# Optimization experiments

Measured on AMD Instinct MI355X. Metric: run time of the kernel, lower is better.

Reference implementation:

```python
import jax, jax.numpy as jnp
import numpy as np

L = 2       # num_layers
D = 256     # d_model
DFF = 1024  # d_ffn
NH = 8      # n_heads
NP = 4      # n_points
CIN = 512   # in_channels
B = 8
HH = 64
WW = 64
EPS = 1e-5


def setup_inputs() -> dict:
    key = jax.random.key(0)
    ks = iter(jax.random.split(key, 48))
    def w(shape, s=0.02):
        return jax.random.normal(next(ks), shape, jnp.float32) * s
    inp = dict(
        x=jax.random.normal(next(ks), (B, CIN, HH, WW), jnp.float32),
        W_in=w((D, CIN)),
        bn1_g=jnp.ones((D,), jnp.float32), bn1_b=jnp.zeros((D,), jnp.float32),
        bn1_m=jnp.zeros((D,), jnp.float32), bn1_v=jnp.ones((D,), jnp.float32),
        query_embed=w((HH * WW, D), 1.0),
        Woff=w((L, D, NH * NP * 2)), boff=w((L, NH * NP * 2), 2.0),
        Wattn=w((L, D, NH * NP)), battn=jnp.zeros((L, NH * NP), jnp.float32),
        Wval=w((L, D, D)), bval=jnp.zeros((L, D), jnp.float32),
        Wo=w((L, D, D)), bo=jnp.zeros((L, D), jnp.float32),
        ln1_g=jnp.ones((L, D), jnp.float32), ln1_b=jnp.zeros((L, D), jnp.float32),
        W1=w((L, D, DFF)), b1=jnp.zeros((L, DFF), jnp.float32),
        W2=w((L, DFF, D)), b2=jnp.zeros((L, D), jnp.float32),
        ln2_g=jnp.ones((L, D), jnp.float32), ln2_b=jnp.zeros((L, D), jnp.float32),
        W_out=w((CIN, D)),
        bn2_g=jnp.ones((CIN,), jnp.float32), bn2_b=jnp.zeros((CIN,), jnp.float32),
        bn2_m=jnp.zeros((CIN,), jnp.float32), bn2_v=jnp.ones((CIN,), jnp.float32),
    )
    return inp


def layer_norm(x, g, b):
    m = jnp.mean(x, axis=-1, keepdims=True)
    v = jnp.mean((x - m) ** 2, axis=-1, keepdims=True)
    return (x - m) * jax.lax.rsqrt(v + EPS) * g + b


def bilinear_sample(value, loc, Hh, Ww):
    # value: (B, NH, dh, H*W); loc: (B, Lq, NH, NP, 2) normalized to [0,1]
    # Matches F.grid_sample(align_corners=False, padding_mode='zeros') with grid=2*loc-1.
    Bn, Lq, nH, P, _ = loc.shape
    gx = loc[..., 0] * Ww - 0.5
    gy = loc[..., 1] * Hh - 0.5
    x0 = jnp.floor(gx)
    y0 = jnp.floor(gy)
    wx = gx - x0
    wy = gy - y0
    x0i = x0.astype(jnp.int32)
    y0i = y0.astype(jnp.int32)

    def t(a):  # (B,Lq,NH,P) -> (B,NH,1,Lq*P)
        return jnp.transpose(a, (0, 2, 1, 3)).reshape(Bn, nH, 1, Lq * P)

    def gather(xi, yi):
        valid = (xi >= 0) & (xi < Ww) & (yi >= 0) & (yi < Hh)
        xc = jnp.clip(xi, 0, Ww - 1)
        yc = jnp.clip(yi, 0, Hh - 1)
        idx = t(yc * Ww + xc)  # (B,NH,1,Lq*P)
        v = jnp.take_along_axis(value, idx, axis=3)  # (B,NH,dh,Lq*P)
        return v * t(valid).astype(value.dtype)

    v00 = gather(x0i, y0i)
    v10 = gather(x0i + 1, y0i)
    v01 = gather(x0i, y0i + 1)
    v11 = gather(x0i + 1, y0i + 1)
    wxt = t(wx)
    wyt = t(wy)
    out = (v00 * (1 - wxt) * (1 - wyt) + v10 * wxt * (1 - wyt)
           + v01 * (1 - wxt) * wyt + v11 * wxt * wyt)
    return out.reshape(Bn, nH, -1, Lq, P)  # (B,NH,dh,Lq,NP)


def reference(x, W_in, bn1_g, bn1_b, bn1_m, bn1_v, query_embed,
              Woff, boff, Wattn, battn, Wval, bval, Wo, bo,
              ln1_g, ln1_b, W1, b1, W2, b2, ln2_g, ln2_b,
              W_out, bn2_g, bn2_b, bn2_m, bn2_v):
    Bn, C, Hh, Ww = x.shape
    HW = Hh * Ww
    dh = D // NH

    # proj_in: 1x1 conv (no bias) + BN (inference) + ReLU
    xp = jnp.einsum('bchw,dc->bdhw', x, W_in)
    xp = (xp - bn1_m[:, None, None]) * jax.lax.rsqrt(bn1_v[:, None, None] + EPS)
    xp = jax.nn.relu(xp * bn1_g[:, None, None] + bn1_b[:, None, None])
    src = xp.reshape(Bn, D, HW).transpose(0, 2, 1)  # (B, HW, D)

    # reference points: centers of pixels, normalized
    ry = (jnp.arange(Hh, dtype=jnp.float32) + 0.5) / Hh
    rx = (jnp.arange(Ww, dtype=jnp.float32) + 0.5) / Ww
    yy, xx = jnp.meshgrid(ry, rx, indexing='ij')
    refpts = jnp.stack([xx, yy], axis=-1).reshape(HW, 2)  # (HW, 2) as (x, y)
    norm = jnp.array([Ww, Hh], jnp.float32)

    q = jnp.broadcast_to(query_embed[None], (Bn, HW, D))
    for i in range(L):
        # --- MSDeformAttn (n_levels=1) ---
        val = (src @ Wval[i] + bval[i]).reshape(Bn, HW, NH, dh)
        val = val.transpose(0, 2, 3, 1)  # (B, NH, dh, HW)
        off = (q @ Woff[i] + boff[i]).reshape(Bn, HW, NH, NP, 2)
        attn = jax.nn.softmax((q @ Wattn[i] + battn[i]).reshape(Bn, HW, NH, NP), axis=-1)
        loc = refpts[None, :, None, None, :] + off / norm  # (B, HW, NH, NP, 2)
        samp = bilinear_sample(val, loc, Hh, Ww)  # (B, NH, dh, HW, NP)
        o = jnp.einsum('bhdqp,bhqp->bqhd', samp, attn.transpose(0, 2, 1, 3))
        o = o.reshape(Bn, HW, D) @ Wo[i] + bo[i]
        q = layer_norm(q + o, ln1_g[i], ln1_b[i])
        # --- FFN ---
        ffn = jax.nn.relu(q @ W1[i] + b1[i]) @ W2[i] + b2[i]
        q = layer_norm(q + ffn, ln2_g[i], ln2_b[i])

    # proj_out: 1x1 conv (no bias) + BN (inference) + ReLU
    y = q.transpose(0, 2, 1).reshape(Bn, D, Hh, Ww)
    y = jnp.einsum('bdhw,cd->bchw', y, W_out)
    y = (y - bn2_m[:, None, None]) * jax.lax.rsqrt(bn2_v[:, None, None] + EPS)
    return jax.nn.relu(y * bn2_g[:, None, None] + bn2_b[:, None, None])
```

## Files before the change

kernel.cpp:

```cpp
#include <hip/hip_runtime.h>
#include <cstdint>

#define LYR 2
#define DM  256
#define DFFN 1024
#define CINC 512
#define BBATCH 8
#define HWTOT 4096
#define EPSV 1e-5f

using u16 = unsigned short;
typedef __attribute__((ext_vector_type(8))) short bf16x8;
typedef __attribute__((ext_vector_type(4))) float f32x4;

__device__ inline u16 f2b(float v) {
    union { float f; uint32_t u; } x; x.f = v;
    uint32_t r = x.u + 0x7fffu + ((x.u >> 16) & 1u);
    return (u16)(r >> 16);
}
__device__ inline uint32_t pk2(float a, float b) {
    return (uint32_t)f2b(a) | ((uint32_t)f2b(b) << 16);
}
__device__ inline float blo(uint32_t d) {
    union { uint32_t i; float f; } x; x.i = d << 16; return x.f;
}
__device__ inline float bhi(uint32_t d) {
    union { uint32_t i; float f; } x; x.i = d & 0xffff0000u; return x.f;
}

template<int MODE>
__global__ __launch_bounds__(256) void mfma_gemm(
    const u16* __restrict__ A, const u16* __restrict__ Bt,
    const float* __restrict__ scale, const float* __restrict__ shift,
    void* __restrict__ Cv, int M, int N, int K, int ldc,
    long long a_zs, long long b_zs, long long c_zs, int swz, int gxlog)
{
    __shared__ u16 As[4][4096];
    __shared__ u16 Bs[4][4096];
    const int tid = threadIdx.x;
    const int lane = tid & 63;
    const int wid = tid >> 6;
    const int wm = (wid & 1) << 6, wn = (wid >> 1) << 6;
    const int quad = lane >> 4, r = lane & 15;

    int bx = blockIdx.x, by = blockIdx.y;
    if (swz) {
        int linear = by * gridDim.x + bx;
        int xcd = linear & 7;
        int s = linear >> 3;
        bx = s & (gridDim.x - 1);
        by = xcd * (gridDim.y >> 3) + (s >> gxlog);
    }
    const int m0 = by << 7, n0 = bx << 7;
    const u16* Ab = A + (long long)blockIdx.z * a_zs + (long long)m0 * K;
    const u16* Bb = Bt + (long long)blockIdx.z * b_zs + (long long)n0 * K;

    const int u0 = tid, u1 = tid + 256;
    const int mu0 = u0 >> 2, cu0 = (u0 & 3) ^ ((mu0 >> 1) & 3);
    const int mu1 = u1 >> 2, cu1 = (u1 & 3) ^ ((mu1 >> 1) & 3);
    const long long ga0 = (long long)mu0 * K + cu0 * 8;
    const long long ga1 = (long long)mu1 * K + cu1 * 8;

    int aoff[4], boff[4];
#pragma unroll
    for (int t = 0; t < 4; ++t) {
        int m = wm + t * 16 + r;
        aoff[t] = (m * 4 + (quad ^ ((m >> 1) & 3))) * 8;
        int n = wn + t * 16 + r;
        boff[t] = (n * 4 + (quad ^ ((n >> 1) & 3))) * 8;
    }

    f32x4 acc[4][4];
#pragma unroll
    for (int i = 0; i < 4; ++i)
#pragma unroll
        for (int j = 0; j < 4; ++j) acc[i][j] = (f32x4){0.f, 0.f, 0.f, 0.f};

    const int NT = K >> 5;

#define GSTAGE(g, b) do {                                                                       \
    const long long kk = (long long)(g) << 5;                                                   \
    __builtin_amdgcn_global_load_lds((const __attribute__((address_space(1))) void*)(Ab + ga0 + kk), \
        (__attribute__((address_space(3))) void*)(&As[b][u0 * 8]), 16, 0, 0);                   \
    __builtin_amdgcn_global_load_lds((const __attribute__((address_space(1))) void*)(Ab + ga1 + kk), \
        (__attribute__((address_space(3))) void*)(&As[b][u1 * 8]), 16, 0, 0);                   \
    __builtin_amdgcn_global_load_lds((const __attribute__((address_space(1))) void*)(Bb + ga0 + kk), \
        (__attribute__((address_space(3))) void*)(&Bs[b][u0 * 8]), 16, 0, 0);                   \
    __builtin_amdgcn_global_load_lds((const __attribute__((address_space(1))) void*)(Bb + ga1 + kk), \
        (__attribute__((address_space(3))) void*)(&Bs[b][u1 * 8]), 16, 0, 0);                   \
} while (0)

    GSTAGE(0, 0);
    GSTAGE(1, 1);
    GSTAGE(2, 2);

    for (int t = 0; t < NT; ++t) {
        if (t < NT - 2)       asm volatile("s_waitcnt vmcnt(8)" ::: "memory");
        else if (t == NT - 2) asm volatile("s_waitcnt vmcnt(4)" ::: "memory");
        else                  asm volatile("s_waitcnt vmcnt(0)" ::: "memory");
        __builtin_amdgcn_s_barrier();
        __builtin_amdgcn_sched_barrier(0);
        if (t + 3 < NT) GSTAGE(t + 3, (t + 3) & 3);
        const u16* Ap = As[t & 3];
        const u16* Bp = Bs[t & 3];
        bf16x8 af[4], bf[4];
#pragma unroll
        for (int tt = 0; tt < 4; ++tt) af[tt] = *(const bf16x8*)(Ap + aoff[tt]);
#pragma unroll
        for (int tt = 0; tt < 4; ++tt) bf[tt] = *(const bf16x8*)(Bp + boff[tt]);
#pragma unroll
        for (int i = 0; i < 4; ++i)
#pragma unroll
            for (int j = 0; j < 4; ++j)
                acc[i][j] = __builtin_amdgcn_mfma_f32_16x16x32_bf16(bf[j], af[i], acc[i][j], 0, 0, 0);
    }
#undef GSTAGE

    const long long zc = (long long)blockIdx.z * c_zs;
    float4 sh4[4], sc4[4];
    if (MODE != 3) {
#pragma unroll
        for (int j = 0; j < 4; ++j) {
            int colb = n0 + wn + j * 16 + quad * 4;
            sh4[j] = *(const float4*)&shift[colb];
            if (MODE == 1) sc4[j] = *(const float4*)&scale[colb];
        }
    }
#pragma unroll
    for (int i = 0; i < 4; ++i) {
        const int row = m0 + wm + i * 16 + r;
        float rsc = 0.f, rsh = 0.f;
        if (MODE == 3) { rsc = scale[row]; rsh = shift[row]; }
#pragma unroll
        for (int j = 0; j < 4; ++j) {
            const int colb = n0 + wn + j * 16 + quad * 4;
            f32x4 v = acc[i][j];
            if (MODE == 0) {
                uint2 o;
                o.x = pk2(v[0] + sh4[j].x, v[1] + sh4[j].y);
                o.y = pk2(v[2] + sh4[j].z, v[3] + sh4[j].w);
                *(uint2*)((u16*)Cv + zc + (long long)row * ldc + colb) = o;
            } else if (MODE == 1) {
                uint2 o;
                o.x = pk2(fmaxf(v[0] * sc4[j].x + sh4[j].x, 0.f), fmaxf(v[1] * sc4[j].y + sh4[j].y, 0.f));
                o.y = pk2(fmaxf(v[2] * sc4[j].z + sh4[j].z, 0.f), fmaxf(v[3] * sc4[j].w + sh4[j].w, 0.f));
                *(uint2*)((u16*)Cv + zc + (long long)row * ldc + colb) = o;
            } else if (MODE == 2) {
                float4 o = {v[0] + sh4[j].x, v[1] + sh4[j].y, v[2] + sh4[j].z, v[3] + sh4[j].w};
                *(float4*)((float*)Cv + zc + (long long)row * ldc + colb) = o;
            } else {
                float4 o = {fmaxf(v[0] * rsc + rsh, 0.f), fmaxf(v[1] * rsc + rsh, 0.f),
                            fmaxf(v[2] * rsc + rsh, 0.f), fmaxf(v[3] * rsc + rsh, 0.f)};
                *(float4*)((float*)Cv + zc + (long long)row * ldc + colb) = o;
            }
        }
    }
}

__global__ __launch_bounds__(512, 4) void mfma_gemm_ln(
    const u16* __restrict__ A, const u16* __restrict__ Bf,
    const float* __restrict__ bias,
    float* __restrict__ q, u16* __restrict__ q16,
    const float* __restrict__ g, const float* __restrict__ beta, int K)
{
    __shared__ u16 As[3][2048];
    __shared__ float red_s[8][64], red_ss[8][64];
    const int tid = threadIdx.x;
    const int lane = tid & 63;
    const int w = tid >> 6;
    const int quad = lane >> 4, r = lane & 15;
    const int m0 = blockIdx.x << 6;
    const u16* Ab = A + (long long)m0 * K;

    const int mA = tid >> 2, cA = (tid & 3) ^ ((mA >> 1) & 3);
    const long long gaA = (long long)mA * K + cA * 8;
    const bool stager = tid < 256;

    int aoff[4];
#pragma unroll
    for (int t = 0; t < 4; ++t) {
        int m = t * 16 + r;
        aoff[t] = (m * 4 + (quad ^ ((m >> 1) & 3))) * 8;
    }

    const u16* Bw = Bf + ((size_t)(2 * w) * 64 + lane) * 8;

    f32x4 acc[4][2];
#pragma unroll
    for (int i = 0; i < 4; ++i)
#pragma unroll
        for (int j = 0; j < 2; ++j) acc[i][j] = (f32x4){0.f, 0.f, 0.f, 0.f};

    const int NT = K >> 5;

    if (stager) {
        __builtin_amdgcn_global_load_lds((const __attribute__((address_space(1))) void*)(Ab + gaA),
                                         (__attribute__((address_space(3))) void*)(&As[0][tid * 8]), 16, 0, 0);
        __builtin_amdgcn_global_load_lds((const __attribute__((address_space(1))) void*)(Ab + gaA + 32),
                                         (__attribute__((address_space(3))) void*)(&As[1][tid * 8]), 16, 0, 0);
    }
    __builtin_amdgcn_sched_barrier(0);
    bf16x8 bc0 = *(const bf16x8*)(Bw);
    bf16x8 bc1 = *(const bf16x8*)(Bw + 512);

    int cb = 0;
    for (int t = 0; t < NT; ++t) {
        asm volatile("s_waitcnt vmcnt(3)" ::: "memory");
        __builtin_amdgcn_s_barrier();
        __builtin_amdgcn_sched_barrier(0);
        int nb = cb + 2; if (nb >= 3) nb -= 3;
        if (stager && t + 2 < NT)
            __builtin_amdgcn_global_load_lds((const __attribute__((address_space(1))) void*)(Ab + gaA + (long long)(t + 2) * 32),
                                             (__attribute__((address_space(3))) void*)(&As[nb][tid * 8]), 16, 0, 0);
        bf16x8 bn0, bn1;
        if (t + 1 < NT) {
            const u16* Bn = Bw + (size_t)(t + 1) * 8192;
            bn0 = *(const bf16x8*)(Bn);
            bn1 = *(const bf16x8*)(Bn + 512);
        } else { bn0 = bc0; bn1 = bc1; }

        const u16* Ac = As[cb];
        bf16x8 af[4];
#pragma unroll
        for (int tt = 0; tt < 4; ++tt) af[tt] = *(const bf16x8*)(Ac + aoff[tt]);
#pragma unroll
        for (int i = 0; i < 4; ++i) {
            acc[i][0] = __builtin_amdgcn_mfma_f32_16x16x32_bf16(bc0, af[i], acc[i][0], 0, 0, 0);
            acc[i][1] = __builtin_amdgcn_mfma_f32_16x16x32_bf16(bc1, af[i], acc[i][1], 0, 0, 0);
        }
        bc0 = bn0; bc1 = bn1;
        cb = (cb + 1 == 3) ? 0 : cb + 1;
    }

    float4 sh2[2];
#pragma unroll
    for (int j = 0; j < 2; ++j)
        sh2[j] = *(const float4*)&bias[w * 32 + j * 16 + quad * 4];

    float s_[4] = {0.f, 0.f, 0.f, 0.f}, ss_[4] = {0.f, 0.f, 0.f, 0.f};
#pragma unroll
    for (int i = 0; i < 4; ++i) {
        const int row = m0 + i * 16 + r;
#pragma unroll
        for (int j = 0; j < 2; ++j) {
            const int colb = w * 32 + j * 16 + quad * 4;
            float4 qo = *(const float4*)&q[(size_t)row * DM + colb];
            acc[i][j][0] += sh2[j].x + qo.x;
            acc[i][j][1] += sh2[j].y + qo.y;
            acc[i][j][2] += sh2[j].z + qo.z;
            acc[i][j][3] += sh2[j].w + qo.w;
#pragma unroll
            for (int e = 0; e < 4; ++e) {
                s_[i] += acc[i][j][e];
                ss_[i] += acc[i][j][e] * acc[i][j][e];
            }
        }
    }
#pragma unroll
    for (int i = 0; i < 4; ++i) {
        s_[i] += __shfl_xor(s_[i], 16);  ss_[i] += __shfl_xor(ss_[i], 16);
        s_[i] += __shfl_xor(s_[i], 32);  ss_[i] += __shfl_xor(ss_[i], 32);
    }
    if (quad == 0) {
#pragma unroll
        for (int i = 0; i < 4; ++i) {
            red_s[w][i * 16 + r] = s_[i];
            red_ss[w][i * 16 + r] = ss_[i];
        }
    }
    __syncthreads();

    float mean[4], rstd[4];
#pragma unroll
    for (int i = 0; i < 4; ++i) {
        float S = 0.f, SS = 0.f;
#pragma unroll
        for (int w2 = 0; w2 < 8; ++w2) { S += red_s[w2][i * 16 + r]; SS += red_ss[w2][i * 16 + r]; }
        mean[i] = S * (1.0f / 256.0f);
        rstd[i] = rsqrtf(SS * (1.0f / 256.0f) - mean[i] * mean[i] + EPSV);
    }

    float4 g4[2], bt4[2];
#pragma unroll
    for (int j = 0; j < 2; ++j) {
        int colb = w * 32 + j * 16 + quad * 4;
        g4[j] = *(const float4*)&g[colb];
        bt4[j] = *(const float4*)&beta[colb];
    }
#pragma unroll
    for (int i = 0; i < 4; ++i) {
        const int row = m0 + i * 16 + r;
#pragma unroll
        for (int j = 0; j < 2; ++j) {
            const int colb = w * 32 + j * 16 + quad * 4;
            float o0 = (acc[i][j][0] - mean[i]) * rstd[i] * g4[j].x + bt4[j].x;
            float o1 = (acc[i][j][1] - mean[i]) * rstd[i] * g4[j].y + bt4[j].y;
            float o2 = (acc[i][j][2] - mean[i]) * rstd[i] * g4[j].z + bt4[j].z;
            float o3 = (acc[i][j][3] - mean[i]) * rstd[i] * g4[j].w + bt4[j].w;
            *(float4*)&q[(size_t)row * DM + colb] = make_float4(o0, o1, o2, o3);
            *(uint2*)(q16 + (size_t)row * DM + colb) = make_uint2(pk2(o0, o1), pk2(o2, o3));
        }
    }
}

__global__ __launch_bounds__(512) void ffn_fused(
    const u16* __restrict__ q16in, const u16* __restrict__ w1F, const u16* __restrict__ w2F,
    const float* __restrict__ b1, const float* __restrict__ b2,
    float* __restrict__ q, u16* __restrict__ q16,
    const float* __restrict__ g, const float* __restrict__ beta)
{
    __shared__ u16 Aq[16384];
    __shared__ u16 hF[16384];
    __shared__ float red_s[8][64], red_ss[8][64];
    const int tid = threadIdx.x;
    const int lane = tid & 63;
    const int w = tid >> 6;
    const int quad = lane >> 4, r = lane & 15;
    const int m0 = blockIdx.x << 6;

    const u16* Ab = q16in + (long long)m0 * DM;
#pragma unroll
    for (int i = 0; i < 4; ++i) {
        int u = tid + i * 512;
        int ks = u >> 8, v = u & 255;
        int m = v >> 2, c = (v & 3) ^ ((m >> 1) & 3);
        __builtin_amdgcn_global_load_lds((const __attribute__((address_space(1))) void*)(Ab + (long long)m * DM + ks * 32 + c * 8),
                                         (__attribute__((address_space(3))) void*)(Aq + u * 8), 16, 0, 0);
    }

    int aoff[4];
#pragma unroll
    for (int t = 0; t < 4; ++t) {
        int m = t * 16 + r;
        aoff[t] = (m * 4 + (quad ^ ((m >> 1) & 3))) * 8;
    }

    f32x4 acc2[4][2];
#pragma unroll
    for (int i = 0; i < 4; ++i)
#pragma unroll
        for (int j = 0; j < 2; ++j) acc2[i][j] = (f32x4){0.f, 0.f, 0.f, 0.f};

    __syncthreads();

    for (int qq = 0; qq < 4; ++qq) {
        f32x4 acc1[4][2];
#pragma unroll
        for (int i = 0; i < 4; ++i)
#pragma unroll
            for (int j = 0; j < 2; ++j) acc1[i][j] = (f32x4){0.f, 0.f, 0.f, 0.f};
        __builtin_amdgcn_s_setprio(1);
#pragma unroll
        for (int ks = 0; ks < 8; ++ks) {
            const u16* bp = w1F + ((size_t)(ks * 64 + qq * 16 + w * 2) * 64 + lane) * 8;
            bf16x8 bf0 = *(const bf16x8*)bp;
            bf16x8 bf1 = *(const bf16x8*)(bp + 512);
            bf16x8 af[4];
#pragma unroll
            for (int t = 0; t < 4; ++t) af[t] = *(const bf16x8*)(Aq + ks * 2048 + aoff[t]);
#pragma unroll
            for (int i = 0; i < 4; ++i) {
                acc1[i][0] = __builtin_amdgcn_mfma_f32_16x16x32_bf16(bf0, af[i], acc1[i][0], 0, 0, 0);
                acc1[i][1] = __builtin_amdgcn_mfma_f32_16x16x32_bf16(bf1, af[i], acc1[i][1], 0, 0, 0);
            }
        }
        __builtin_amdgcn_s_setprio(0);
        __syncthreads();

#pragma unroll
        for (int j = 0; j < 2; ++j) {
            const int cb = qq * 256 + w * 32 + j * 16 + quad * 4;
            const float4 b14 = *(const float4*)&b1[cb];
            const int lane2 = r | (((j * 2 + (quad >> 1)) & 3) << 4);
            const int eo = (quad & 1) * 4;
#pragma unroll
            for (int i = 0; i < 4; ++i) {
                f32x4 v = acc1[i][j];
                uint2 o;
                o.x = pk2(fmaxf(v[0] + b14.x, 0.f), fmaxf(v[1] + b14.y, 0.f));
                o.y = pk2(fmaxf(v[2] + b14.z, 0.f), fmaxf(v[3] + b14.w, 0.f));
                *(uint2*)(hF + ((w * 4 + i) * 64 + lane2) * 8 + eo) = o;
            }
        }
        __syncthreads();

        __builtin_amdgcn_s_setprio(1);
#pragma unroll
        for (int ks = 0; ks < 8; ++ks) {
            const u16* bp = w2F + ((size_t)((qq * 8 + ks) * 16 + w * 2) * 64 + lane) * 8;
            bf16x8 bf0 = *(const bf16x8*)bp;
            bf16x8 bf1 = *(const bf16x8*)(bp + 512);
            bf16x8 af[4];
#pragma unroll
            for (int t = 0; t < 4; ++t) af[t] = *(const bf16x8*)(hF + ((ks * 4 + t) * 64 + lane) * 8);
#pragma unroll
            for (int i = 0; i < 4; ++i) {
                acc2[i][0] = __builtin_amdgcn_mfma_f32_16x16x32_bf16(bf0, af[i], acc2[i][0], 0, 0, 0);
                acc2[i][1] = __builtin_amdgcn_mfma_f32_16x16x32_bf16(bf1, af[i], acc2[i][1], 0, 0, 0);
            }
        }
        __builtin_amdgcn_s_setprio(0);
    }

    float4 sh2[2];
#pragma unroll
    for (int j = 0; j < 2; ++j)
        sh2[j] = *(const float4*)&b2[w * 32 + j * 16 + quad * 4];

    float s_[4] = {0.f, 0.f, 0.f, 0.f}, ss_[4] = {0.f, 0.f, 0.f, 0.f};
#pragma unroll
    for (int i = 0; i < 4; ++i) {
        const int row = m0 + i * 16 + r;
#pragma unroll
        for (int j = 0; j < 2; ++j) {
            const int colb = w * 32 + j * 16 + quad * 4;
            float4 qo = *(const float4*)&q[(size_t)row * DM + colb];
            acc2[i][j][0] += sh2[j].x + qo.x;
            acc2[i][j][1] += sh2[j].y + qo.y;
            acc2[i][j][2] += sh2[j].z + qo.z;
            acc2[i][j][3] += sh2[j].w + qo.w;
#pragma unroll
            for (int e = 0; e < 4; ++e) {
                s_[i] += acc2[i][j][e];
                ss_[i] += acc2[i][j][e] * acc2[i][j][e];
            }
        }
    }
#pragma unroll
    for (int i = 0; i < 4; ++i) {
        s_[i] += __shfl_xor(s_[i], 16);  ss_[i] += __shfl_xor(ss_[i], 16);
        s_[i] += __shfl_xor(s_[i], 32);  ss_[i] += __shfl_xor(ss_[i], 32);
    }
    if (quad == 0) {
#pragma unroll
        for (int i = 0; i < 4; ++i) {
            red_s[w][i * 16 + r] = s_[i];
            red_ss[w][i * 16 + r] = ss_[i];
        }
    }
    __syncthreads();

    float mean[4], rstd[4];
#pragma unroll
    for (int i = 0; i < 4; ++i) {
        float S = 0.f, SS = 0.f;
#pragma unroll
        for (int w2 = 0; w2 < 8; ++w2) { S += red_s[w2][i * 16 + r]; SS += red_ss[w2][i * 16 + r]; }
        mean[i] = S * (1.0f / 256.0f);
        rstd[i] = rsqrtf(SS * (1.0f / 256.0f) - mean[i] * mean[i] + EPSV);
    }

    float4 g4[2], bt4[2];
#pragma unroll
    for (int j = 0; j < 2; ++j) {
        int colb = w * 32 + j * 16 + quad * 4;
        g4[j] = *(const float4*)&g[colb];
        bt4[j] = *(const float4*)&beta[colb];
    }
#pragma unroll
    for (int i = 0; i < 4; ++i) {
        const int row = m0 + i * 16 + r;
#pragma unroll
        for (int j = 0; j < 2; ++j) {
            const int colb = w * 32 + j * 16 + quad * 4;
            float o0 = (acc2[i][j][0] - mean[i]) * rstd[i] * g4[j].x + bt4[j].x;
            float o1 = (acc2[i][j][1] - mean[i]) * rstd[i] * g4[j].y + bt4[j].y;
            float o2 = (acc2[i][j][2] - mean[i]) * rstd[i] * g4[j].z + bt4[j].z;
            float o3 = (acc2[i][j][3] - mean[i]) * rstd[i] * g4[j].w + bt4[j].w;
            *(float4*)&q[(size_t)row * DM + colb] = make_float4(o0, o1, o2, o3);
            *(uint2*)(q16 + (size_t)row * DM + colb) = make_uint2(pk2(o0, o1), pk2(o2, o3));
        }
    }
}

__device__ __attribute__((noinline)) void tconv(const float* src, u16* dst, int K, int N, int tk, int tn)
{
    __shared__ float t[32][33];
    const int tx = threadIdx.x & 31, ty = threadIdx.x >> 5;
#pragma unroll
    for (int i = 0; i < 4; ++i)
        t[ty + i * 8][tx] = src[(size_t)(tk * 32 + ty + i * 8) * N + tn * 32 + tx];
    __syncthreads();
#pragma unroll
    for (int i = 0; i < 4; ++i)
        dst[(size_t)(tn * 32 + ty + i * 8) * K + tk * 32 + tx] = f2b(t[tx][ty + i * 8]);
}

__device__ __attribute__((noinline)) void tconv_oa(const float* Woff, const float* Wattn, u16* dst, int tk, int tn)
{
    __shared__ float t[32][33];
    const int tx = threadIdx.x & 31, ty = threadIdx.x >> 5;
#pragma unroll
    for (int i = 0; i < 4; ++i) {
        int k = tk * 32 + ty + i * 8, n = tn * 32 + tx;
        float v = (n < 64) ? Woff[k * 64 + n] : ((n < 96) ? Wattn[k * 32 + n - 64] : 0.f);
        t[ty + i * 8][tx] = v;
    }
    __syncthreads();
#pragma unroll
    for (int i = 0; i < 4; ++i)
        dst[(size_t)(tn * 32 + ty + i * 8) * 256 + tk * 32 + tx] = f2b(t[tx][ty + i * 8]);
}

__device__ __attribute__((noinline)) void frag_prep(const float* W, u16* dst, int ks, int nc, int N)
{
    __shared__ float t[32][256];
    const int tid = threadIdx.x;
#pragma unroll
    for (int kk = 0; kk < 32; ++kk)
        t[kk][tid] = W[(size_t)(ks * 32 + kk) * N + nc * 256 + tid];
    __syncthreads();
    const int NT16 = N >> 4;
#pragma unroll
    for (int i = 0; i < 4; ++i) {
        int idx = tid + i * 256;
        int nt = idx >> 6, l = idx & 63;
        int n = nt * 16 + (l & 15);
        int kb = (l >> 4) * 8;
        u16 o[8];
#pragma unroll
        for (int e = 0; e < 8; ++e) o[e] = f2b(t[kb + e][n]);
        *(uint4*)(dst + ((size_t)(ks * NT16 + nc * 16 + nt) * 64 + l) * 8) = *(const uint4*)o;
    }
}

__global__ __launch_bounds__(256) void prep_weights(
    const float* __restrict__ Wval, const float* __restrict__ Wo,
    const float* __restrict__ W1, const float* __restrict__ W2,
    const float* __restrict__ Woff, const float* __restrict__ Wattn,
    const float* __restrict__ boff, const float* __restrict__ battn,
    const float* __restrict__ W_in, const float* __restrict__ W_out,
    const float* __restrict__ bn1g, const float* __restrict__ bn1b,
    const float* __restrict__ bn1m, const float* __restrict__ bn1v,
    const float* __restrict__ bn2g, const float* __restrict__ bn2b,
    const float* __restrict__ bn2m, const float* __restrict__ bn2v,
    u16* __restrict__ wvalT, u16* __restrict__ woF, u16* __restrict__ w1F,
    u16* __restrict__ w2F, u16* __restrict__ woaT,
    u16* __restrict__ winC, u16* __restrict__ woutC,
    float* __restrict__ bn1sc, float* __restrict__ bn1sh,
    float* __restrict__ bn2sc, float* __restrict__ bn2sh, float* __restrict__ boa)
{
    int bid = blockIdx.x;
    if (bid < 128) {
        int l = bid >> 6, r2 = bid & 63;
        tconv(Wval + l * 65536, wvalT + l * 65536, 256, 256, r2 & 7, r2 >> 3);
    } else if (bid < 192) {
        int i2 = bid - 128, l = i2 >> 5, r2 = i2 & 31;
        tconv_oa(Woff + l * 16384, Wattn + l * 8192, woaT + l * 32768, r2 & 7, r2 >> 3);
    } else if (bid < 208) {
        int i2 = bid - 192;
        frag_prep(Wo + (i2 >> 3) * 65536, woF + (i2 >> 3) * 65536, i2 & 7, 0, 256);
    } else if (bid < 272) {
        int i2 = bid - 208, l = i2 >> 5, r2 = i2 & 31;
        frag_prep(W1 + l * 262144, w1F + l * 262144, r2 >> 2, r2 & 3, 1024);
    } else if (bid < 336) {
        int i2 = bid - 272;
        frag_prep(W2 + (i2 >> 5) * 262144, w2F + (i2 >> 5) * 262144, i2 & 31, 0, 256);
    } else if (bid < 368) {
        int g2 = bid - 336, base = g2 * 4096, t = threadIdx.x;
#pragma unroll
        for (int k = 0; k < 16; ++k) winC[base + k * 256 + t] = f2b(W_in[base + k * 256 + t]);
    } else if (bid < 400) {
        int g2 = bid - 368, base = g2 * 4096, t = threadIdx.x;
#pragma unroll
        for (int k = 0; k < 16; ++k) woutC[base + k * 256 + t] = f2b(W_out[base + k * 256 + t]);
    } else {
        int t = threadIdx.x;
        { float s = bn1g[t] * rsqrtf(bn1v[t] + EPSV); bn1sc[t] = s; bn1sh[t] = bn1b[t] - bn1m[t] * s; }
        for (int c = 0; c < 2; ++c) {
            int i = c * 256 + t;
            float s = bn2g[i] * rsqrtf(bn2v[i] + EPSV);
            bn2sc[i] = s; bn2sh[i] = bn2b[i] - bn2m[i] * s;
        }
        if (t < 128)
            for (int l = 0; l < 2; ++l)
                boa[l * 128 + t] = (t < 64) ? boff[l * 64 + t]
                                 : ((t < 96) ? battn[l * 32 + t - 64] : 0.f);
    }
}

__global__ __launch_bounds__(256) void transpose_x(const float* __restrict__ x, u16* __restrict__ xT)
{
    __shared__ float t[64][65];
    const int b = blockIdx.z, p0 = blockIdx.y << 6, c0 = blockIdx.x << 6;
    const int tx = threadIdx.x & 63, ty = threadIdx.x >> 6;
    const float* xb = x + ((size_t)b * CINC + c0) * HWTOT + p0;
#pragma unroll
    for (int i = 0; i < 16; ++i)
        t[ty + i * 4][tx] = xb[(size_t)(ty + i * 4) * HWTOT + tx];
    __syncthreads();
    u16* xo = xT + ((size_t)b * HWTOT + p0) * CINC + c0;
#pragma unroll
    for (int i = 0; i < 16; ++i)
        xo[(size_t)(ty + i * 4) * CINC + tx] = f2b(t[tx][ty + i * 4]);
}

struct IW { int eo; float w; };

__global__ __launch_bounds__(256) void sample_kernel(
    const u16* __restrict__ val,
    const float* __restrict__ oa,
    u16* __restrict__ oms)
{
    __shared__ float s_oa[8][96];
    __shared__ IW s_iw[8][32][5];
    const int t = threadIdx.x;
    const int bq0 = blockIdx.x << 3;
    const int b = blockIdx.x >> 9;

    {
        int qi = t >> 5, j = t & 31;
        if (j < 24)
            ((float4*)s_oa[qi])[j] = ((const float4*)oa)[((size_t)(bq0 + qi)) * 32 + j];
    }
    __syncthreads();

    {
        const int qi = t >> 5, hp = t & 31, h = hp >> 2, p = hp & 3;
        const float* so = s_oa[qi];
        float l0 = so[64 + h * 4 + 0], l1 = so[64 + h * 4 + 1];
        float l2 = so[64 + h * 4 + 2], l3 = so[64 + h * 4 + 3];
        float mx = fmaxf(fmaxf(l0, l1), fmaxf(l2, l3));
        float e0 = __expf(l0 - mx), e1 = __expf(l1 - mx), e2 = __expf(l2 - mx), e3 = __expf(l3 - mx);
        float inv = 1.0f / (e0 + e1 + e2 + e3);
        float aw = ((p == 0) ? e0 : (p == 1) ? e1 : (p == 2) ? e2 : e3) * inv;
        const int bq = bq0 + qi;
        float gx = (float)(bq & 63) + so[hp * 2 + 0];
        float gy = (float)((bq >> 6) & 63) + so[hp * 2 + 1];
        float x0f = floorf(gx), y0f = floorf(gy);
        float wx = gx - x0f, wy = gy - y0f;
        int x0 = (int)x0f, y0 = (int)y0f;
#pragma unroll
        for (int c = 0; c < 4; ++c) {
            int xi = x0 + (c & 1), yi = y0 + (c >> 1);
            bool ok = (xi >= 0) && (xi < 64) && (yi >= 0) && (yi < 64);
            float wgt = ((c & 1) ? wx : 1.0f - wx) * ((c >> 1) ? wy : 1.0f - wy);
            s_iw[qi][hp][c].eo = ok ? ((yi * 64 + xi) << 8) : 0;
            s_iw[qi][hp][c].w = ok ? aw * wgt : 0.f;
        }
    }
    __syncthreads();

    {
        const int qi = t >> 5, l = t & 31, h = l >> 2, cc = l & 3;
        const u16* base = val + ((size_t)b << 20) + (h << 5) + (cc << 3);
        float a[8] = {0.f, 0.f, 0.f, 0.f, 0.f, 0.f, 0.f, 0.f};
#pragma unroll
        for (int p = 0; p < 4; ++p)
#pragma unroll
            for (int c = 0; c < 4; ++c) {
                IW iw = s_iw[qi][(h << 2) + p][c];
                uint4 v = *(const uint4*)(base + iw.eo);
                a[0] += iw.w * blo(v.x); a[1] += iw.w * bhi(v.x);
                a[2] += iw.w * blo(v.y); a[3] += iw.w * bhi(v.y);
                a[4] += iw.w * blo(v.z); a[5] += iw.w * bhi(v.z);
                a[6] += iw.w * blo(v.w); a[7] += iw.w * bhi(v.w);
            }
        uint4 o;
        o.x = (uint32_t)f2b(a[0]) | ((uint32_t)f2b(a[1]) << 16);
        o.y = (uint32_t)f2b(a[2]) | ((uint32_t)f2b(a[3]) << 16);
        o.z = (uint32_t)f2b(a[4]) | ((uint32_t)f2b(a[5]) << 16);
        o.w = (uint32_t)f2b(a[6]) | ((uint32_t)f2b(a[7]) << 16);
        *(uint4*)(oms + (size_t)(bq0 + qi) * 256 + (h << 5) + (cc << 3)) = o;
    }
}

__global__ __launch_bounds__(256) void bcast_q(
    const float4* __restrict__ qe, float4* __restrict__ q, u16* __restrict__ q16)
{
    const int i = blockIdx.x * 256 + threadIdx.x;
    float4 v = qe[i];
    uint2 pk = make_uint2(pk2(v.x, v.y), pk2(v.z, v.w));
#pragma unroll
    for (int b = 0; b < BBATCH; ++b) {
        q[(size_t)b * 262144 + i] = v;
        ((uint2*)q16)[(size_t)b * 262144 + i] = pk;
    }
}

extern "C" void kernel_launch(void* const* d_in, const int* in_sizes, int n_in,
                              void* d_out, int out_size, void* d_ws, size_t ws_size,
                              hipStream_t stream)
{
    (void)in_sizes; (void)n_in; (void)out_size; (void)ws_size;
    const float* x     = (const float*)d_in[0];
    const float* W_in  = (const float*)d_in[1];
    const float* bn1_g = (const float*)d_in[2];
    const float* bn1_b = (const float*)d_in[3];
    const float* bn1_m = (const float*)d_in[4];
    const float* bn1_v = (const float*)d_in[5];
    const float* qe    = (const float*)d_in[6];
    const float* Woff  = (const float*)d_in[7];
    const float* boff  = (const float*)d_in[8];
    const float* Wattn = (const float*)d_in[9];
    const float* battn = (const float*)d_in[10];
    const float* Wval  = (const float*)d_in[11];
    const float* bval  = (const float*)d_in[12];
    const float* Wo    = (const float*)d_in[13];
    const float* bo    = (const float*)d_in[14];
    const float* ln1_g = (const float*)d_in[15];
    const float* ln1_b = (const float*)d_in[16];
    const float* W1    = (const float*)d_in[17];
    const float* b1    = (const float*)d_in[18];
    const float* W2    = (const float*)d_in[19];
    const float* b2    = (const float*)d_in[20];
    const float* ln2_g = (const float*)d_in[21];
    const float* ln2_b = (const float*)d_in[22];
    const float* W_out = (const float*)d_in[23];
    const float* bn2_g = (const float*)d_in[24];
    const float* bn2_b = (const float*)d_in[25];
    const float* bn2_m = (const float*)d_in[26];
    const float* bn2_v = (const float*)d_in[27];
    float* out = (float*)d_out;

    char* w = (char*)d_ws;
    char* pool    = w;          w += 67108864;
    float* q      = (float*)w;  w += 33554432;
    u16*  q16     = (u16*)w;    w += 16777216;
    u16*  src16   = (u16*)w;    w += 16777216;
    u16*  wvalT   = (u16*)w;    w += 262144;
    u16*  woF     = (u16*)w;    w += 262144;
    u16*  w1F     = (u16*)w;    w += 1048576;
    u16*  w2F     = (u16*)w;    w += 1048576;
    u16*  woaT    = (u16*)w;    w += 131072;
    u16*  winC    = (u16*)w;    w += 262144;
    u16*  woutC   = (u16*)w;    w += 262144;
    float* bn1sc  = (float*)w;  w += 1024;
    float* bn1sh  = (float*)w;  w += 1024;
    float* bn2sc  = (float*)w;  w += 2048;
    float* bn2sh  = (float*)w;  w += 2048;
    float* boa    = (float*)w;  w += 1024;

    u16*  xT     = (u16*)pool;
    u16*  val16  = (u16*)pool;
    float* offat = (float*)(pool + 16777216);
    u16*  oms16  = (u16*)(pool + 33554432);

    prep_weights<<<dim3(401), 256, 0, stream>>>(
        Wval, Wo, W1, W2, Woff, Wattn, boff, battn, W_in, W_out,
        bn1_g, bn1_b, bn1_m, bn1_v, bn2_g, bn2_b, bn2_m, bn2_v,
        wvalT, woF, w1F, w2F, woaT, winC, woutC, bn1sc, bn1sh, bn2sc, bn2sh, boa);
    transpose_x<<<dim3(CINC / 64, HWTOT / 64, BBATCH), 256, 0, stream>>>(x, xT);
    bcast_q<<<dim3(1024), 256, 0, stream>>>((const float4*)qe, (float4*)q, q16);

    mfma_gemm<1><<<dim3(2, 256, 1), 256, 0, stream>>>(
        xT, winC, bn1sc, bn1sh, src16, 32768, 256, 512, 256, 0, 0, 0, 1, 1);

    for (int l = 0; l < LYR; ++l) {
        mfma_gemm<0><<<dim3(2, 256, 1), 256, 0, stream>>>(
            src16, wvalT + l * 65536, nullptr, bval + l * 256, val16,
            32768, 256, 256, 256, 0, 0, 0, 1, 1);
        mfma_gemm<2><<<dim3(1, 256, 1), 256, 0, stream>>>(
            q16, woaT + l * 32768, nullptr, boa + l * 128, offat,
            32768, 128, 256, 128, 0, 0, 0, 1, 0);
        sample_kernel<<<dim3(4096), 256, 0, stream>>>(val16, offat, oms16);
        mfma_gemm_ln<<<dim3(512), 512, 0, stream>>>(
            oms16, woF + l * 65536, bo + l * 256, q, q16,
            ln1_g + l * 256, ln1_b + l * 256, 256);
        ffn_fused<<<dim3(512), 512, 0, stream>>>(
            q16, w1F + l * 262144, w2F + l * 262144,
            b1 + l * 1024, b2 + l * 256, q, q16,
            ln2_g + l * 256, ln2_b + l * 256);
    }

    mfma_gemm<3><<<dim3(32, 4, BBATCH), 256, 0, stream>>>(
        woutC, q16, bn2sc, bn2sh, out, 512, 4096, 256, 4096,
        0, (long long)HWTOT * DM, (long long)CINC * HWTOT, 0, 0);
}
```

Before: 458.1 us.

## Fuse output projection, LayerNorm1 and FFN with LayerNorm2 into one kernel

Merges the Wo GEMM + residual + LayerNorm kernel with the FFN + LayerNorm kernel into a single per-64-row-tile kernel. The LN1 output is written as bf16 directly into shared memory for the FFN's first GEMM and kept in registers as the residual, so the q/q16 write and reread between the two kernels and one launch per layer go away. The first FFN GEMM is split per 16-column half to reduce register pressure, and the shared buffer for the attention output is reused for the hidden activations. The Wo GEMM loses its pipelined triple-buffered loading, and the larger shared footprint may reduce occupancy.

```diff
diff --git a/kernel.cpp b/kernel.cpp
--- a/kernel.cpp
+++ b/kernel.cpp
@@ -157,24 +157,32 @@
     }
 }
 
-__global__ __launch_bounds__(512, 4) void mfma_gemm_ln(
-    const u16* __restrict__ A, const u16* __restrict__ Bf,
-    const float* __restrict__ bias,
+__global__ __launch_bounds__(512, 4) void fused_layer(
+    const u16* __restrict__ oms, const u16* __restrict__ woF,
+    const u16* __restrict__ w1F, const u16* __restrict__ w2F,
+    const float* __restrict__ bo, const float* __restrict__ b1, const float* __restrict__ b2,
     float* __restrict__ q, u16* __restrict__ q16,
-    const float* __restrict__ g, const float* __restrict__ beta, int K)
-{
-    __shared__ u16 As[3][2048];
+    const float* __restrict__ g1, const float* __restrict__ be1,
+    const float* __restrict__ g2, const float* __restrict__ be2)
+{
+    __shared__ u16 AqO[16384];
+    __shared__ u16 AqQ[16384];
     __shared__ float red_s[8][64], red_ss[8][64];
     const int tid = threadIdx.x;
     const int lane = tid & 63;
     const int w = tid >> 6;
     const int quad = lane >> 4, r = lane & 15;
     const int m0 = blockIdx.x << 6;
-    const u16* Ab = A + (long long)m0 * K;
-
-    const int mA = tid >> 2, cA = (tid & 3) ^ ((mA >> 1) & 3);
-    const long long gaA = (long long)mA * K + cA * 8;
-    const bool stager = tid < 256;
+
+    const u16* Ab = oms + (long long)m0 * DM;
+#pragma unroll
+    for (int i = 0; i < 4; ++i) {
+        int u = tid + i * 512;
+        int ks = u >> 8, v = u & 255;
+        int m = v >> 2, c = (v & 3) ^ ((m >> 1) & 3);
+        __builtin_amdgcn_global_load_lds((const __attribute__((address_space(1))) void*)(Ab + (long long)m * DM + ks * 32 + c * 8),
+                                         (__attribute__((address_space(3))) void*)(AqO + u * 8), 16, 0, 0);
+    }
 
     int aoff[4];
 #pragma unroll
@@ -183,59 +191,33 @@
         aoff[t] = (m * 4 + (quad ^ ((m >> 1) & 3))) * 8;
     }
 
-    const u16* Bw = Bf + ((size_t)(2 * w) * 64 + lane) * 8;
-
     f32x4 acc[4][2];
 #pragma unroll
     for (int i = 0; i < 4; ++i)
 #pragma unroll
         for (int j = 0; j < 2; ++j) acc[i][j] = (f32x4){0.f, 0.f, 0.f, 0.f};
 
-    const int NT = K >> 5;
-
-    if (stager) {
-        __builtin_amdgcn_global_load_lds((const __attribute__((address_space(1))) void*)(Ab + gaA),
-                                         (__attribute__((address_space(3))) void*)(&As[0][tid * 8]), 16, 0, 0);
-        __builtin_amdgcn_global_load_lds((const __attribute__((address_space(1))) void*)(Ab + gaA + 32),
-                                         (__attribute__((address_space(3))) void*)(&As[1][tid * 8]), 16, 0, 0);
-    }
-    __builtin_amdgcn_sched_barrier(0);
-    bf16x8 bc0 = *(const bf16x8*)(Bw);
-    bf16x8 bc1 = *(const bf16x8*)(Bw + 512);
-
-    int cb = 0;
-    for (int t = 0; t < NT; ++t) {
-        asm volatile("s_waitcnt vmcnt(3)" ::: "memory");
-        __builtin_amdgcn_s_barrier();
-        __builtin_amdgcn_sched_barrier(0);
-        int nb = cb + 2; if (nb >= 3) nb -= 3;
-        if (stager && t + 2 < NT)
-            __builtin_amdgcn_global_load_lds((const __attribute__((address_space(1))) void*)(Ab + gaA + (long long)(t + 2) * 32),
-                                             (__attribute__((address_space(3))) void*)(&As[nb][tid * 8]), 16, 0, 0);
-        bf16x8 bn0, bn1;
-        if (t + 1 < NT) {
-            const u16* Bn = Bw + (size_t)(t + 1) * 8192;
-            bn0 = *(const bf16x8*)(Bn);
-            bn1 = *(const bf16x8*)(Bn + 512);
-        } else { bn0 = bc0; bn1 = bc1; }
-
-        const u16* Ac = As[cb];
+    __syncthreads();
+
+#pragma unroll
+    for (int ks = 0; ks < 8; ++ks) {
+        const u16* bp = woF + ((size_t)(ks * 16 + 2 * w) * 64 + lane) * 8;
+        bf16x8 bf0 = *(const bf16x8*)bp;
+        bf16x8 bf1 = *(const bf16x8*)(bp + 512);
         bf16x8 af[4];
 #pragma unroll
-        for (int tt = 0; tt < 4; ++tt) af[tt] = *(const bf16x8*)(Ac + aoff[tt]);
+        for (int t = 0; t < 4; ++t) af[t] = *(const bf16x8*)(AqO + ks * 2048 + aoff[t]);
 #pragma unroll
         for (int i = 0; i < 4; ++i) {
-            acc[i][0] = __builtin_amdgcn_mfma_f32_16x16x32_bf16(bc0, af[i], acc[i][0], 0, 0, 0);
-            acc[i][1] = __builtin_amdgcn_mfma_f32_16x16x32_bf16(bc1, af[i], acc[i][1], 0, 0, 0);
-        }
-        bc0 = bn0; bc1 = bn1;
-        cb = (cb + 1 == 3) ? 0 : cb + 1;
+            acc[i][0] = __builtin_amdgcn_mfma_f32_16x16x32_bf16(bf0, af[i], acc[i][0], 0, 0, 0);
+            acc[i][1] = __builtin_amdgcn_mfma_f32_16x16x32_bf16(bf1, af[i], acc[i][1], 0, 0, 0);
+        }
     }
 
     float4 sh2[2];
 #pragma unroll
     for (int j = 0; j < 2; ++j)
-        sh2[j] = *(const float4*)&bias[w * 32 + j * 16 + quad * 4];
+        sh2[j] = *(const float4*)&bo[w * 32 + j * 16 + quad * 4];
 
     float s_[4] = {0.f, 0.f, 0.f, 0.f}, ss_[4] = {0.f, 0.f, 0.f, 0.f};
 #pragma unroll
@@ -280,60 +262,32 @@
         rstd[i] = rsqrtf(SS * (1.0f / 256.0f) - mean[i] * mean[i] + EPSV);
     }
 
-    float4 g4[2], bt4[2];
-#pragma unroll
-    for (int j = 0; j < 2; ++j) {
-        int colb = w * 32 + j * 16 + quad * 4;
-        g4[j] = *(const float4*)&g[colb];
-        bt4[j] = *(const float4*)&beta[colb];
-    }
-#pragma unroll
-    for (int i = 0; i < 4; ++i) {
-        const int row = m0 + i * 16 + r;
+    f32x4 oreg[4][2];
+    {
+        float4 g4[2], bt4[2];
 #pragma unroll
         for (int j = 0; j < 2; ++j) {
-            const int colb = w * 32 + j * 16 + quad * 4;
-            float o0 = (acc[i][j][0] - mean[i]) * rstd[i] * g4[j].x + bt4[j].x;
-            float o1 = (acc[i][j][1] - mean[i]) * rstd[i] * g4[j].y + bt4[j].y;
-            float o2 = (acc[i][j][2] - mean[i]) * rstd[i] * g4[j].z + bt4[j].z;
-            float o3 = (acc[i][j][3] - mean[i]) * rstd[i] * g4[j].w + bt4[j].w;
-            *(float4*)&q[(size_t)row * DM + colb] = make_float4(o0, o1, o2, o3);
-            *(uint2*)(q16 + (size_t)row * DM + colb) = make_uint2(pk2(o0, o1), pk2(o2, o3));
-        }
-    }
-}
-
-__global__ __launch_bounds__(512) void ffn_fused(
-    const u16* __restrict__ q16in, const u16* __restrict__ w1F, const u16* __restrict__ w2F,
-    const float* __restrict__ b1, const float* __restrict__ b2,
-    float* __restrict__ q, u16* __restrict__ q16,
-    const float* __restrict__ g, const float* __restrict__ beta)
-{
-    __shared__ u16 Aq[16384];
-    __shared__ u16 hF[16384];
-    __shared__ float red_s[8][64], red_ss[8][64];
-    const int tid = threadIdx.x;
-    const int lane = tid & 63;
-    const int w = tid >> 6;
-    const int quad = lane >> 4, r = lane & 15;
-    const int m0 = blockIdx.x << 6;
-
-    const u16* Ab = q16in + (long long)m0 * DM;
-#pragma unroll
-    for (int i = 0; i < 4; ++i) {
-        int u = tid + i * 512;
-        int ks = u >> 8, v = u & 255;
-        int m = v >> 2, c = (v & 3) ^ ((m >> 1) & 3);
-        __builtin_amdgcn_global_load_lds((const __attribute__((address_space(1))) void*)(Ab + (long long)m * DM + ks * 32 + c * 8),
-                                         (__attribute__((address_space(3))) void*)(Aq + u * 8), 16, 0, 0);
-    }
-
-    int aoff[4];
-#pragma unroll
-    for (int t = 0; t < 4; ++t) {
-        int m = t * 16 + r;
-        aoff[t] = (m * 4 + (quad ^ ((m >> 1) & 3))) * 8;
-    }
+            int colb = w * 32 + j * 16 + quad * 4;
+            g4[j] = *(const float4*)&g1[colb];
+            bt4[j] = *(const float4*)&be1[colb];
+        }
+#pragma unroll
+        for (int i = 0; i < 4; ++i) {
+            const int mm = i * 16 + r;
+#pragma unroll
+            for (int j = 0; j < 2; ++j) {
+                float o0 = (acc[i][j][0] - mean[i]) * rstd[i] * g4[j].x + bt4[j].x;
+                float o1 = (acc[i][j][1] - mean[i]) * rstd[i] * g4[j].y + bt4[j].y;
+                float o2 = (acc[i][j][2] - mean[i]) * rstd[i] * g4[j].z + bt4[j].z;
+                float o3 = (acc[i][j][3] - mean[i]) * rstd[i] * g4[j].w + bt4[j].w;
+                oreg[i][j] = (f32x4){o0, o1, o2, o3};
+                const int pp = (j * 2 + (quad >> 1)) ^ ((r >> 1) & 3);
+                *(uint2*)(AqQ + w * 2048 + (mm * 4 + pp) * 8 + (quad & 1) * 4) =
+                    make_uint2(pk2(o0, o1), pk2(o2, o3));
+            }
+        }
+    }
+    __syncthreads();
 
     f32x4 acc2[4][2];
 #pragma unroll
@@ -341,45 +295,37 @@
 #pragma unroll
         for (int j = 0; j < 2; ++j) acc2[i][j] = (f32x4){0.f, 0.f, 0.f, 0.f};
 
-    __syncthreads();
-
     for (int qq = 0; qq < 4; ++qq) {
-        f32x4 acc1[4][2];
-#pragma unroll
-        for (int i = 0; i < 4; ++i)
-#pragma unroll
-            for (int j = 0; j < 2; ++j) acc1[i][j] = (f32x4){0.f, 0.f, 0.f, 0.f};
-        __builtin_amdgcn_s_setprio(1);
-#pragma unroll
-        for (int ks = 0; ks < 8; ++ks) {
-            const u16* bp = w1F + ((size_t)(ks * 64 + qq * 16 + w * 2) * 64 + lane) * 8;
-            bf16x8 bf0 = *(const bf16x8*)bp;
-            bf16x8 bf1 = *(const bf16x8*)(bp + 512);
-            bf16x8 af[4];
-#pragma unroll
-            for (int t = 0; t < 4; ++t) af[t] = *(const bf16x8*)(Aq + ks * 2048 + aoff[t]);
-#pragma unroll
-            for (int i = 0; i < 4; ++i) {
-                acc1[i][0] = __builtin_amdgcn_mfma_f32_16x16x32_bf16(bf0, af[i], acc1[i][0], 0, 0, 0);
-                acc1[i][1] = __builtin_amdgcn_mfma_f32_16x16x32_bf16(bf1, af[i], acc1[i][1], 0, 0, 0);
+        if (qq) __syncthreads();
+#pragma unroll
+        for (int j = 0; j < 2; ++j) {
+            f32x4 a1[4];
+#pragma unroll
+            for (int i = 0; i < 4; ++i) a1[i] = (f32x4){0.f, 0.f, 0.f, 0.f};
+            __builtin_amdgcn_s_setprio(1);
+#pragma unroll
+            for (int ks = 0; ks < 8; ++ks) {
+                const u16* bp = w1F + ((size_t)(ks * 64 + qq * 16 + w * 2 + j) * 64 + lane) * 8;
+                bf16x8 bf = *(const bf16x8*)bp;
+                bf16x8 af[4];
+#pragma unroll
+                for (int t = 0; t < 4; ++t) af[t] = *(const bf16x8*)(AqQ + ks * 2048 + aoff[t]);
+#pragma unroll
+                for (int i = 0; i < 4; ++i)
+                    a1[i] = __builtin_amdgcn_mfma_f32_16x16x32_bf16(bf, af[i], a1[i], 0, 0, 0);
             }
-        }
-        __builtin_amdgcn_s_setprio(0);
-        __syncthreads();
-
-#pragma unroll
-        for (int j = 0; j < 2; ++j) {
+            __builtin_amdgcn_s_setprio(0);
             const int cb = qq * 256 + w * 32 + j * 16 + quad * 4;
             const float4 b14 = *(const float4*)&b1[cb];
             const int lane2 = r | (((j * 2 + (quad >> 1)) & 3) << 4);
             const int eo = (quad & 1) * 4;
 #pragma unroll
             for (int i = 0; i < 4; ++i) {
-                f32x4 v = acc1[i][j];
+                f32x4 v = a1[i];
                 uint2 o;
                 o.x = pk2(fmaxf(v[0] + b14.x, 0.f), fmaxf(v[1] + b14.y, 0.f));
                 o.y = pk2(fmaxf(v[2] + b14.z, 0.f), fmaxf(v[3] + b14.w, 0.f));
-                *(uint2*)(hF + ((w * 4 + i) * 64 + lane2) * 8 + eo) = o;
+                *(uint2*)(AqO + ((w * 4 + i) * 64 + lane2) * 8 + eo) = o;
             }
         }
         __syncthreads();
@@ -392,7 +338,7 @@
             bf16x8 bf1 = *(const bf16x8*)(bp + 512);
             bf16x8 af[4];
 #pragma unroll
-            for (int t = 0; t < 4; ++t) af[t] = *(const bf16x8*)(hF + ((ks * 4 + t) * 64 + lane) * 8);
+            for (int t = 0; t < 4; ++t) af[t] = *(const bf16x8*)(AqO + ((ks * 4 + t) * 64 + lane) * 8);
 #pragma unroll
             for (int i = 0; i < 4; ++i) {
                 acc2[i][0] = __builtin_amdgcn_mfma_f32_16x16x32_bf16(bf0, af[i], acc2[i][0], 0, 0, 0);
@@ -402,23 +348,20 @@
         __builtin_amdgcn_s_setprio(0);
     }
 
-    float4 sh2[2];
 #pragma unroll
     for (int j = 0; j < 2; ++j)
         sh2[j] = *(const float4*)&b2[w * 32 + j * 16 + quad * 4];
 
-    float s_[4] = {0.f, 0.f, 0.f, 0.f}, ss_[4] = {0.f, 0.f, 0.f, 0.f};
-#pragma unroll
-    for (int i = 0; i < 4; ++i) {
-        const int row = m0 + i * 16 + r;
+#pragma unroll
+    for (int i = 0; i < 4; ++i) { s_[i] = 0.f; ss_[i] = 0.f; }
+#pragma unroll
+    for (int i = 0; i < 4; ++i) {
 #pragma unroll
         for (int j = 0; j < 2; ++j) {
-            const int colb = w * 32 + j * 16 + quad * 4;
-            float4 qo = *(const float4*)&q[(size_t)row * DM + colb];
-            acc2[i][j][0] += sh2[j].x + qo.x;
-            acc2[i][j][1] += sh2[j].y + qo.y;
-            acc2[i][j][2] += sh2[j].z + qo.z;
-            acc2[i][j][3] += sh2[j].w + qo.w;
+            acc2[i][j][0] += sh2[j].x + oreg[i][j][0];
+            acc2[i][j][1] += sh2[j].y + oreg[i][j][1];
+            acc2[i][j][2] += sh2[j].z + oreg[i][j][2];
+            acc2[i][j][3] += sh2[j].w + oreg[i][j][3];
 #pragma unroll
             for (int e = 0; e < 4; ++e) {
                 s_[i] += acc2[i][j][e];
@@ -440,7 +383,6 @@
     }
     __syncthreads();
 
-    float mean[4], rstd[4];
 #pragma unroll
     for (int i = 0; i < 4; ++i) {
         float S = 0.f, SS = 0.f;
@@ -454,8 +396,8 @@
 #pragma unroll
     for (int j = 0; j < 2; ++j) {
         int colb = w * 32 + j * 16 + quad * 4;
-        g4[j] = *(const float4*)&g[colb];
-        bt4[j] = *(const float4*)&beta[colb];
+        g4[j] = *(const float4*)&g2[colb];
+        bt4[j] = *(const float4*)&be2[colb];
     }
 #pragma unroll
     for (int i = 0; i < 4; ++i) {
@@ -754,13 +696,10 @@
             q16, woaT + l * 32768, nullptr, boa + l * 128, offat,
             32768, 128, 256, 128, 0, 0, 0, 1, 0);
         sample_kernel<<<dim3(4096), 256, 0, stream>>>(val16, offat, oms16);
-        mfma_gemm_ln<<<dim3(512), 512, 0, stream>>>(
-            oms16, woF + l * 65536, bo + l * 256, q, q16,
-            ln1_g + l * 256, ln1_b + l * 256, 256);
-        ffn_fused<<<dim3(512), 512, 0, stream>>>(
-            q16, w1F + l * 262144, w2F + l * 262144,
-            b1 + l * 1024, b2 + l * 256, q, q16,
-            ln2_g + l * 256, ln2_b + l * 256);
+        fused_layer<<<dim3(512), 512, 0, stream>>>(
+            oms16, woF + l * 65536, w1F + l * 262144, w2F + l * 262144,
+            bo + l * 256, b1 + l * 1024, b2 + l * 256, q, q16,
+            ln1_g + l * 256, ln1_b + l * 256, ln2_g + l * 256, ln2_b + l * 256);
     }
 
     mfma_gemm<3><<<dim3(32, 4, BBATCH), 256, 0, stream>>>(
```

Measured after the change: 461.3 us. No clear change (+0.7%).
